# Kernel tuning notes

Hardware: AMD Instinct MI355X
Metric: run time of the kernel (lower is better)

The kernel has to match this reference:

```python
import jax, jax.numpy as jnp
import numpy as np

SQ, SK, B, H, D = 2048, 2048, 2, 16, 64
LAYER_NUMBER = 1  # coeff for query_key_layer_scaling
MASK_FILL = -10000.0  # attention_mask_func fill value


def setup_inputs() -> dict:
    key = jax.random.key(0)
    kq, kk, kv = jax.random.split(key, 3)
    query_layer = jax.random.normal(kq, (SQ, B, H, D), dtype=jnp.float32)
    key_layer = jax.random.normal(kk, (SK, B, H, D), dtype=jnp.float32)
    value_layer = jax.random.normal(kv, (SK, B, H, D), dtype=jnp.float32)
    attention_mask = jnp.zeros((B, 1, SQ, SK), dtype=bool)  # ignored for causal mask type
    return {
        "query_layer": query_layer,
        "key_layer": key_layer,
        "value_layer": value_layer,
        "attention_mask": attention_mask,
    }


def reference(query_layer, key_layer, value_layer, attention_mask):
    sq, b, h, d = query_layer.shape
    sk = key_layer.shape[0]
    coeff = float(LAYER_NUMBER)
    norm_factor = np.sqrt(d) * coeff  # norm_factor = sqrt(d) * layer_number

    # BMM1: [b,h,sq,sk] scores, scaled by 1/norm_factor
    scores = jnp.einsum("sbhd,tbhd->bhst", query_layer, key_layer) / norm_factor

    # FusedScaleMaskSoftmax: scale by coeff in fp32, causal mask, softmax
    scores = scores.astype(jnp.float32) * coeff
    causal = jnp.triu(jnp.ones((sq, sk), dtype=bool), k=1)  # True above diagonal -> masked
    scores = jnp.where(causal[None, None], MASK_FILL, scores)
    probs = jax.nn.softmax(scores, axis=-1).astype(query_layer.dtype)

    # dropout p=0.0 -> identity

    # BMM2: context [sq,b,h,d] -> [sq,b,h*d]
    context = jnp.einsum("bhst,tbhd->sbhd", probs, value_layer)
    return context.reshape(sq, b, h * d)
```

## Files before the change

kernel.cpp:

```cpp
#include <hip/hip_runtime.h>

typedef short bf16x8 __attribute__((ext_vector_type(8)));
typedef float f32x4 __attribute__((ext_vector_type(4)));
typedef unsigned u32x4 __attribute__((ext_vector_type(4)));
typedef unsigned u32x2 __attribute__((ext_vector_type(2)));
typedef unsigned short ushort_t;

#define RS 2048
#define LDSK 72
#define PSTR 40
#define QSCALE 0.18033688011f
#define BH_STRIDE (2048*64)

static __device__ __forceinline__ unsigned pkbf(float a, float b) {
    union { float f; unsigned u; } ua, ub; ua.f = a; ub.f = b;
    return ((ua.u + 0x8000u) >> 16) | ((ub.u + 0x8000u) & 0xffff0000u);
}

static __device__ __forceinline__ float fexp2(float x) {
#if __has_builtin(__builtin_amdgcn_exp2f)
    return __builtin_amdgcn_exp2f(x);
#else
    return exp2f(x);
#endif
}

static __device__ __forceinline__ void gload16(const ushort_t* g, short* l) {
    __builtin_amdgcn_global_load_lds(
        (const __attribute__((address_space(1))) unsigned int*)(g),
        (__attribute__((address_space(3))) unsigned int*)(l), 16, 0, 0);
}

__global__ __launch_bounds__(256)
void prep_bf16(const float* __restrict__ K, const float* __restrict__ V,
               ushort_t* __restrict__ Kbf, ushort_t* __restrict__ Vtb)
{
    __shared__ short Tt[64 * LDSK];
    const int kt = blockIdx.x, bh = blockIdx.y;
    const int t = threadIdx.x;

    {
        const int key = t >> 2, cq = (t & 3) * 16;
        const float* kp = K + (size_t)(kt * 64 + key) * RS + bh * 64 + cq;
        f32x4 a0 = *(const f32x4*)kp,     a1 = *(const f32x4*)(kp + 4);
        f32x4 a2 = *(const f32x4*)(kp + 8), a3 = *(const f32x4*)(kp + 12);
        u32x4 w0, w1;
        w0[0] = pkbf(a0[0], a0[1]); w0[1] = pkbf(a0[2], a0[3]);
        w0[2] = pkbf(a1[0], a1[1]); w0[3] = pkbf(a1[2], a1[3]);
        w1[0] = pkbf(a2[0], a2[1]); w1[1] = pkbf(a2[2], a2[3]);
        w1[2] = pkbf(a3[0], a3[1]); w1[3] = pkbf(a3[2], a3[3]);
        ushort_t* kout = Kbf + (size_t)bh * BH_STRIDE + (size_t)(kt * 64 + key) * 64 + cq;
        *(u32x4*)kout = w0;
        *(u32x4*)(kout + 8) = w1;
    }
    {
        const int vkey = (t & 31) * 2, vd = (t >> 5) * 8;
        const float* vp = V + (size_t)(kt * 64 + vkey) * RS + bh * 64 + vd;
        f32x4 b0 = *(const f32x4*)vp,        b1 = *(const f32x4*)(vp + 4);
        f32x4 c0 = *(const f32x4*)(vp + RS), c1 = *(const f32x4*)(vp + RS + 4);
        #pragma unroll
        for (int i = 0; i < 4; ++i) {
            *(unsigned*)&Tt[(vd + i) * LDSK + vkey]     = pkbf(b0[i], c0[i]);
            *(unsigned*)&Tt[(vd + 4 + i) * LDSK + vkey] = pkbf(b1[i], c1[i]);
        }
    }
    __syncthreads();
    {
        const int d = t >> 2, kq = (t & 3) * 16;
        ushort_t* vout = Vtb + (size_t)bh * BH_STRIDE + (size_t)d * RS + kt * 64 + kq;
        u32x4 w0 = *(const u32x4*)&Tt[d * LDSK + kq];
        u32x4 w1 = *(const u32x4*)&Tt[d * LDSK + kq + 8];
        *(u32x4*)vout = w0;
        *(u32x4*)(vout + 8) = w1;
    }
}

__global__ __launch_bounds__(256, 4)
void fa_fwd3(const float* __restrict__ Q, const ushort_t* __restrict__ Kbf,
             const ushort_t* __restrict__ Vtb, float* __restrict__ Out)
{
    __shared__ alignas(16) short Kd[2][4096];
    __shared__ alignas(16) short Vd[2][4096];
    __shared__ alignas(16) short Psh[4][16 * PSTR];

    const int x = blockIdx.x;
    const int chunk = x >> 8, idx = x & 255;
    const int bh = idx & 31, s = idx >> 5;
    const int qt = (chunk == 0) ? (31 - s) : (chunk == 1) ? (23 - s)
                 : (chunk == 2) ? s : (8 + s);
    const int base = bh * 64;
    const int tid = threadIdx.x;
    const int wave = tid >> 6;
    const int n15 = tid & 15, quad = (tid & 63) >> 4;
    const int q0 = qt * 64;

    const int srow = tid >> 3, sg = (tid & 7) ^ (srow & 7);
    const ushort_t* kb2 = Kbf + (size_t)bh * BH_STRIDE + srow * 64 + sg * 8;
    const ushort_t* vb2 = Vtb + (size_t)bh * BH_STRIDE + (size_t)srow * RS + sg * 8;

    auto stage = [&](int buf, int kt) {
        const ushort_t* ks = kb2 + (size_t)kt * 4096;
        const ushort_t* vs = vb2 + kt * 64;
        short* kd = &Kd[buf][wave * 512];
        short* vd = &Vd[buf][wave * 512];
        gload16(ks,         kd);
        gload16(ks + 2048,  kd + 2048);
        gload16(vs,         vd);
        gload16(vs + 65536, vd + 2048);
    };

    stage(0, 0);

    bf16x8 qf[2];
    {
        const float* qp = Q + (size_t)(q0 + wave * 16 + n15) * RS + base + quad * 8;
        #pragma unroll
        for (int ks = 0; ks < 2; ++ks) {
            f32x4 a0 = *(const f32x4*)(qp + ks * 32) * QSCALE;
            f32x4 a1 = *(const f32x4*)(qp + ks * 32 + 4) * QSCALE;
            union { u32x4 u; bf16x8 s; } w;
            w.u[0] = pkbf(a0[0], a0[1]); w.u[1] = pkbf(a0[2], a0[3]);
            w.u[2] = pkbf(a1[0], a1[1]); w.u[3] = pkbf(a1[2], a1[3]);
            qf[ks] = w.s;
        }
    }

    f32x4 O[4];
    #pragma unroll
    for (int i = 0; i < 4; ++i) O[i] = (f32x4){0.f, 0.f, 0.f, 0.f};
    float l = 0.f;

    const int c0 = (quad * 8) ^ ((n15 & 7) * 8);
    const int c1 = c0 ^ 32;

    asm volatile("s_waitcnt vmcnt(0)" ::: "memory");
    __builtin_amdgcn_sched_barrier(0);
    __builtin_amdgcn_s_barrier();

    int buf = 0;
    for (int kt = 0; kt <= qt; ++kt) {
        if (kt < qt) stage(buf ^ 1, kt + 1);
        const short* Kb_ = Kd[buf];
        const short* Vb_ = Vd[buf];

        f32x4 S[4];
        __builtin_amdgcn_s_setprio(1);
        #pragma unroll
        for (int mb = 0; mb < 4; ++mb) {
            const short* kr = Kb_ + (mb * 16 + n15) * 64;
            bf16x8 kf0 = *(const bf16x8*)(kr + c0);
            bf16x8 kf1 = *(const bf16x8*)(kr + c1);
            f32x4 sv = (f32x4){0.f, 0.f, 0.f, 0.f};
            sv = __builtin_amdgcn_mfma_f32_16x16x32_bf16(kf0, qf[0], sv, 0, 0, 0);
            sv = __builtin_amdgcn_mfma_f32_16x16x32_bf16(kf1, qf[1], sv, 0, 0, 0);
            S[mb] = sv;
        }
        __builtin_amdgcn_s_setprio(0);

        if (kt == qt) {
            const int kb_ = kt * 64;
            const int q = q0 + wave * 16 + n15;
            #pragma unroll
            for (int mb = 0; mb < 4; ++mb)
                #pragma unroll
                for (int r = 0; r < 4; ++r)
                    if (kb_ + mb * 16 + quad * 4 + r > q) S[mb][r] = -1e30f;
        }

        float rs = 0.f;
        bf16x8 pf[2];
        #pragma unroll
        for (int half = 0; half < 2; ++half) {
            #pragma unroll
            for (int m2 = 0; m2 < 2; ++m2) {
                f32x4 sv = S[half * 2 + m2];
                float p0 = fexp2(sv[0]), p1 = fexp2(sv[1]);
                float p2 = fexp2(sv[2]), p3 = fexp2(sv[3]);
                rs += (p0 + p1) + (p2 + p3);
                unsigned w0, w1;
                asm("v_cvt_pk_bf16_f32 %0, %1, %2" : "=v"(w0) : "v"(p0), "v"(p1));
                asm("v_cvt_pk_bf16_f32 %0, %1, %2" : "=v"(w1) : "v"(p2), "v"(p3));
                u32x2 w; w[0] = w0; w[1] = w1;
                *(u32x2*)&Psh[wave][n15 * PSTR + m2 * 16 + quad * 4] = w;
            }
            pf[half] = *(const bf16x8*)&Psh[wave][n15 * PSTR + quad * 8];
        }
        rs += __shfl_xor(rs, 16);
        rs += __shfl_xor(rs, 32);
        l += rs;

        __builtin_amdgcn_s_setprio(1);
        #pragma unroll
        for (int db = 0; db < 4; ++db) {
            const short* vr = Vb_ + (db * 16 + n15) * 64;
            bf16x8 vf0 = *(const bf16x8*)(vr + c0);
            O[db] = __builtin_amdgcn_mfma_f32_16x16x32_bf16(pf[0], vf0, O[db], 0, 0, 0);
            bf16x8 vf1 = *(const bf16x8*)(vr + c1);
            O[db] = __builtin_amdgcn_mfma_f32_16x16x32_bf16(pf[1], vf1, O[db], 0, 0, 0);
        }
        __builtin_amdgcn_s_setprio(0);

        if (kt < qt) {
            asm volatile("s_waitcnt vmcnt(0)" ::: "memory");
            __builtin_amdgcn_sched_barrier(0);
            __builtin_amdgcn_s_barrier();
            buf ^= 1;
        }
    }

    #pragma unroll
    for (int r = 0; r < 4; ++r) {
        float inv = 1.0f / __shfl(l, quad * 4 + r);
        size_t row = (size_t)(q0 + wave * 16 + quad * 4 + r) * RS + base;
        #pragma unroll
        for (int db = 0; db < 4; ++db)
            Out[row + db * 16 + n15] = O[db][r] * inv;
    }
}

__global__ __launch_bounds__(256, 3)
void fa_fwd_fb(const float* __restrict__ Q, const float* __restrict__ K,
               const float* __restrict__ V, float* __restrict__ Out)
{
    __shared__ short Ksh[2][64 * LDSK];
    __shared__ short Vt[2][64 * LDSK];
    __shared__ short Psh[4][16 * LDSK];

    const int qt = 31 - blockIdx.y;
    const int bh = blockIdx.x;
    const int base = bh * 64;
    const int tid = threadIdx.x;
    const int wave = tid >> 6, lane = tid & 63;
    const int n15 = lane & 15, quad = lane >> 4;
    const int q0 = qt * 64;
    const int krow = tid >> 2, kcg = (tid & 3) * 16;
    const int vkey = (tid & 31) * 2, vd = (tid >> 5) * 4;

    bf16x8 qf[2];
    {
        const float* qp = Q + (size_t)(q0 + wave * 16 + n15) * RS + base + quad * 8;
        #pragma unroll
        for (int ks = 0; ks < 2; ++ks) {
            f32x4 a0 = *(const f32x4*)(qp + ks * 32) * QSCALE;
            f32x4 a1 = *(const f32x4*)(qp + ks * 32 + 4) * QSCALE;
            union { u32x4 u; bf16x8 s; } w;
            w.u[0] = pkbf(a0[0], a0[1]); w.u[1] = pkbf(a0[2], a0[3]);
            w.u[2] = pkbf(a1[0], a1[1]); w.u[3] = pkbf(a1[2], a1[3]);
            qf[ks] = w.s;
        }
    }
    f32x4 O[4];
    #pragma unroll
    for (int i = 0; i < 4; ++i) O[i] = (f32x4){0.f, 0.f, 0.f, 0.f};
    float l = 0.f;
    f32x4 rk0, rk1, rk2, rk3, rv0, rv1, rv2, rv3;
    auto prefetch = [&](int kt) {
        const int kb = kt * 64;
        const float* kp = K + (size_t)(kb + krow) * RS + base + kcg;
        rk0 = *(const f32x4*)kp;       rk1 = *(const f32x4*)(kp + 4);
        rk2 = *(const f32x4*)(kp + 8); rk3 = *(const f32x4*)(kp + 12);
        const float* vp = V + (size_t)(kb + vkey) * RS + base + vd;
        rv0 = *(const f32x4*)vp;        rv1 = *(const f32x4*)(vp + RS);
        rv2 = *(const f32x4*)(vp + 32); rv3 = *(const f32x4*)(vp + RS + 32);
    };
    auto stage = [&](int buf) {
        u32x4 w0; w0[0] = pkbf(rk0[0], rk0[1]); w0[1] = pkbf(rk0[2], rk0[3]);
                  w0[2] = pkbf(rk1[0], rk1[1]); w0[3] = pkbf(rk1[2], rk1[3]);
        *(u32x4*)&Ksh[buf][krow * LDSK + kcg] = w0;
        u32x4 w1; w1[0] = pkbf(rk2[0], rk2[1]); w1[1] = pkbf(rk2[2], rk2[3]);
                  w1[2] = pkbf(rk3[0], rk3[1]); w1[3] = pkbf(rk3[2], rk3[3]);
        *(u32x4*)&Ksh[buf][krow * LDSK + kcg + 8] = w1;
        #pragma unroll
        for (int i = 0; i < 4; ++i) {
            *(unsigned*)&Vt[buf][(vd + i) * LDSK + vkey] = pkbf(rv0[i], rv1[i]);
            *(unsigned*)&Vt[buf][(vd + 32 + i) * LDSK + vkey] = pkbf(rv2[i], rv3[i]);
        }
    };
    auto compute = [&](int buf, int kb, bool diag) {
        f32x4 S[4];
        #pragma unroll
        for (int mb = 0; mb < 4; ++mb) {
            f32x4 sv = (f32x4){0.f, 0.f, 0.f, 0.f};
            bf16x8 kf0 = *(const bf16x8*)&Ksh[buf][(mb * 16 + n15) * LDSK + quad * 8];
            sv = __builtin_amdgcn_mfma_f32_16x16x32_bf16(kf0, qf[0], sv, 0, 0, 0);
            bf16x8 kf1 = *(const bf16x8*)&Ksh[buf][(mb * 16 + n15) * LDSK + 32 + quad * 8];
            sv = __builtin_amdgcn_mfma_f32_16x16x32_bf16(kf1, qf[1], sv, 0, 0, 0);
            S[mb] = sv;
        }
        if (diag) {
            int q = q0 + wave * 16 + n15;
            #pragma unroll
            for (int mb = 0; mb < 4; ++mb)
                #pragma unroll
                for (int r = 0; r < 4; ++r)
                    if (kb + mb * 16 + quad * 4 + r > q) S[mb][r] = -1e30f;
        }
        float rs = 0.f;
        #pragma unroll
        for (int mb = 0; mb < 4; ++mb) {
            float p0 = fexp2(S[mb][0]), p1 = fexp2(S[mb][1]);
            float p2 = fexp2(S[mb][2]), p3 = fexp2(S[mb][3]);
            rs += (p0 + p1) + (p2 + p3);
            u32x2 w; w[0] = pkbf(p0, p1); w[1] = pkbf(p2, p3);
            *(u32x2*)&Psh[wave][n15 * LDSK + mb * 16 + quad * 4] = w;
        }
        rs += __shfl_xor(rs, 16);
        rs += __shfl_xor(rs, 32);
        l += rs;
        bf16x8 pf0 = *(const bf16x8*)&Psh[wave][n15 * LDSK + quad * 8];
        bf16x8 pf1 = *(const bf16x8*)&Psh[wave][n15 * LDSK + 32 + quad * 8];
        #pragma unroll
        for (int db = 0; db < 4; ++db) {
            bf16x8 vf0 = *(const bf16x8*)&Vt[buf][(db * 16 + n15) * LDSK + quad * 8];
            O[db] = __builtin_amdgcn_mfma_f32_16x16x32_bf16(pf0, vf0, O[db], 0, 0, 0);
            bf16x8 vf1 = *(const bf16x8*)&Vt[buf][(db * 16 + n15) * LDSK + 32 + quad * 8];
            O[db] = __builtin_amdgcn_mfma_f32_16x16x32_bf16(pf1, vf1, O[db], 0, 0, 0);
        }
    };
    prefetch(0);
    stage(0);
    __syncthreads();
    for (int kt = 0; kt <= qt; ++kt) {
        const int cur = kt & 1;
        if (kt < qt) prefetch(kt + 1);
        compute(cur, kt * 64, kt == qt);
        if (kt < qt) stage(1 - cur);
        __syncthreads();
    }
    #pragma unroll
    for (int r = 0; r < 4; ++r) {
        float inv = 1.0f / __shfl(l, quad * 4 + r);
        size_t row = (size_t)(q0 + wave * 16 + quad * 4 + r) * RS + base;
        #pragma unroll
        for (int db = 0; db < 4; ++db)
            Out[row + db * 16 + n15] = O[db][r] * inv;
    }
}

extern "C" void kernel_launch(void* const* d_in, const int* in_sizes, int n_in,
                              void* d_out, int out_size, void* d_ws, size_t ws_size,
                              hipStream_t stream) {
    const float* Q = (const float*)d_in[0];
    const float* K = (const float*)d_in[1];
    const float* V = (const float*)d_in[2];
    float* Out = (float*)d_out;

    if (ws_size >= (size_t)2 * 32 * BH_STRIDE * sizeof(ushort_t)) {
        ushort_t* Kbf = (ushort_t*)d_ws;
        ushort_t* Vtb = Kbf + (size_t)32 * BH_STRIDE;
        prep_bf16<<<dim3(32, 32), dim3(256), 0, stream>>>(K, V, Kbf, Vtb);
        fa_fwd3<<<dim3(1024), dim3(256), 0, stream>>>(Q, Kbf, Vtb, Out);
    } else {
        fa_fwd_fb<<<dim3(32, 32), dim3(256), 0, stream>>>(Q, K, V, Out);
    }
}
```

Measured before the change: 141.2 us.

## Split long causal query tiles across two KV halves with combine kernel

Query tiles 16-31 are now split into two blocks, each covering half of the causal KV range. The blocks write unnormalized partial outputs and row sums to workspace, and a new combine kernel sums and normalizes them. This shortens the longest blocks and evens out the tail of the work across 1536 blocks. The cost is an extra launch, extra global traffic for the partials, and a larger workspace requirement, which could push execution onto the fallback path if the workspace is too small. Because softmax here uses no running max, the two partials can simply be added.

```diff
diff --git a/kernel.cpp b/kernel.cpp
--- a/kernel.cpp
+++ b/kernel.cpp
@@ -76,18 +76,37 @@
 }
 
 __global__ __launch_bounds__(256, 4)
-void fa_fwd3(const float* __restrict__ Q, const ushort_t* __restrict__ Kbf,
-             const ushort_t* __restrict__ Vtb, float* __restrict__ Out)
+void fa_fwd4(const float* __restrict__ Q, const ushort_t* __restrict__ Kbf,
+             const ushort_t* __restrict__ Vtb, float* __restrict__ Out,
+             float* __restrict__ pO, float* __restrict__ pL)
 {
     __shared__ alignas(16) short Kd[2][4096];
     __shared__ alignas(16) short Vd[2][4096];
     __shared__ alignas(16) short Psh[4][16 * PSTR];
 
     const int x = blockIdx.x;
-    const int chunk = x >> 8, idx = x & 255;
-    const int bh = idx & 31, s = idx >> 5;
-    const int qt = (chunk == 0) ? (31 - s) : (chunk == 1) ? (23 - s)
-                 : (chunk == 2) ? s : (8 + s);
+    int qt, bh, kt0, kt1, pslot = 0;
+    bool hasdiag, direct;
+    if (x < 512) {
+        const int i = x; qt = 31 - (i >> 6); bh = (i >> 1) & 31;
+        const int half = i & 1, mid = (qt + 1) >> 1;
+        kt0 = half ? mid : 0; kt1 = half ? qt : (mid - 1);
+        hasdiag = half; direct = false;
+        pslot = ((qt - 16) * 32 + bh) * 2 + half;
+    } else if (x < 768) {
+        const int i = x - 512; qt = 15 - (i >> 5); bh = i & 31;
+        kt0 = 0; kt1 = qt; hasdiag = true; direct = true;
+    } else if (x < 1280) {
+        const int i = x - 768; qt = 23 - (i >> 6); bh = (i >> 1) & 31;
+        const int half = i & 1, mid = (qt + 1) >> 1;
+        kt0 = half ? mid : 0; kt1 = half ? qt : (mid - 1);
+        hasdiag = half; direct = false;
+        pslot = ((qt - 16) * 32 + bh) * 2 + half;
+    } else {
+        const int i = x - 1280; qt = 7 - (i >> 5); bh = i & 31;
+        kt0 = 0; kt1 = qt; hasdiag = true; direct = true;
+    }
+
     const int base = bh * 64;
     const int tid = threadIdx.x;
     const int wave = tid >> 6;
@@ -109,7 +128,7 @@
         gload16(vs + 65536, vd + 2048);
     };
 
-    stage(0, 0);
+    stage(0, kt0);
 
     bf16x8 qf[2];
     {
@@ -138,8 +157,8 @@
     __builtin_amdgcn_s_barrier();
 
     int buf = 0;
-    for (int kt = 0; kt <= qt; ++kt) {
-        if (kt < qt) stage(buf ^ 1, kt + 1);
+    for (int kt = kt0; kt <= kt1; ++kt) {
+        if (kt < kt1) stage(buf ^ 1, kt + 1);
         const short* Kb_ = Kd[buf];
         const short* Vb_ = Vd[buf];
 
@@ -157,7 +176,7 @@
         }
         __builtin_amdgcn_s_setprio(0);
 
-        if (kt == qt) {
+        if (hasdiag && kt == qt) {
             const int kb_ = kt * 64;
             const int q = q0 + wave * 16 + n15;
             #pragma unroll
@@ -200,7 +219,7 @@
         }
         __builtin_amdgcn_s_setprio(0);
 
-        if (kt < qt) {
+        if (kt < kt1) {
             asm volatile("s_waitcnt vmcnt(0)" ::: "memory");
             __builtin_amdgcn_sched_barrier(0);
             __builtin_amdgcn_s_barrier();
@@ -208,13 +227,45 @@
         }
     }
 
+    if (direct) {
+        #pragma unroll
+        for (int r = 0; r < 4; ++r) {
+            float inv = 1.0f / __shfl(l, quad * 4 + r);
+            size_t row = (size_t)(q0 + wave * 16 + quad * 4 + r) * RS + base;
+            #pragma unroll
+            for (int db = 0; db < 4; ++db)
+                Out[row + db * 16 + n15] = O[db][r] * inv;
+        }
+    } else {
+        float* po = pO + (size_t)pslot * 4096;
+        #pragma unroll
+        for (int r = 0; r < 4; ++r) {
+            const int row = wave * 16 + quad * 4 + r;
+            #pragma unroll
+            for (int db = 0; db < 4; ++db)
+                po[row * 64 + db * 16 + n15] = O[db][r];
+        }
+        if (quad == 0) pL[pslot * 64 + wave * 16 + n15] = l;
+    }
+}
+
+__global__ __launch_bounds__(256)
+void fa_combine(const float* __restrict__ pO, const float* __restrict__ pL,
+                float* __restrict__ Out)
+{
+    const int pair = blockIdx.x;
+    const int qt = 16 + (pair >> 5), bh = pair & 31;
+    const int tid = threadIdx.x;
+    const int r = tid >> 2, c = (tid & 3) * 16;
+    const float* a = pO + (size_t)(pair * 2) * 4096 + r * 64 + c;
+    const float* b = a + 4096;
+    const float inv = 1.0f / (pL[(pair * 2) * 64 + r] + pL[(pair * 2 + 1) * 64 + r]);
+    float* o = Out + (size_t)(qt * 64 + r) * RS + bh * 64 + c;
     #pragma unroll
-    for (int r = 0; r < 4; ++r) {
-        float inv = 1.0f / __shfl(l, quad * 4 + r);
-        size_t row = (size_t)(q0 + wave * 16 + quad * 4 + r) * RS + base;
-        #pragma unroll
-        for (int db = 0; db < 4; ++db)
-            Out[row + db * 16 + n15] = O[db][r] * inv;
+    for (int j = 0; j < 4; ++j) {
+        f32x4 va = ((const f32x4*)a)[j];
+        f32x4 vb = ((const f32x4*)b)[j];
+        ((f32x4*)o)[j] = (va + vb) * inv;
     }
 }
 
@@ -345,11 +396,18 @@
     const float* V = (const float*)d_in[2];
     float* Out = (float*)d_out;
 
-    if (ws_size >= (size_t)2 * 32 * BH_STRIDE * sizeof(ushort_t)) {
+    const size_t kv_bytes = (size_t)2 * 32 * BH_STRIDE * sizeof(ushort_t);
+    const size_t po_bytes = (size_t)1024 * 4096 * sizeof(float);
+    const size_t pl_bytes = (size_t)1024 * 64 * sizeof(float);
+
+    if (ws_size >= kv_bytes + po_bytes + pl_bytes) {
         ushort_t* Kbf = (ushort_t*)d_ws;
         ushort_t* Vtb = Kbf + (size_t)32 * BH_STRIDE;
+        float* pO = (float*)((char*)d_ws + kv_bytes);
+        float* pL = pO + (size_t)1024 * 4096;
         prep_bf16<<<dim3(32, 32), dim3(256), 0, stream>>>(K, V, Kbf, Vtb);
-        fa_fwd3<<<dim3(1024), dim3(256), 0, stream>>>(Q, Kbf, Vtb, Out);
+        fa_fwd4<<<dim3(1536), dim3(256), 0, stream>>>(Q, Kbf, Vtb, Out, pO, pL);
+        fa_combine<<<dim3(512), dim3(256), 0, stream>>>(pO, pL, Out);
     } else {
         fa_fwd_fb<<<dim3(32, 32), dim3(256), 0, stream>>>(Q, K, V, Out);
     }
```

After: 152.1 us. +7.8%, slower.
